# Kernel tuning notes

Measured on AMD Instinct MI355X. Metric: run time of the kernel, lower is better.

## Reference

```python
import jax, jax.numpy as jnp
import numpy as np

N = 50000      # neurons
R = 10         # max receptors per neuron
D = 5          # max delay (steps)
E = 10000000   # recurrent synapses
B = 1          # batch
DT = 1.0
LR_SCALE = 1.0
REC_DAMP = 0.4       # recurrent_dampening_factor
DAMPENING = 0.3      # dampening_factor (surrogate grad)


def setup_inputs() -> dict:
    key = jax.random.key(0)
    ks = jax.random.split(key, 20)
    inputs = jax.random.normal(ks[0], (B, R * N), jnp.float32) * 0.01
    z_buf = (jax.random.uniform(ks[1], (B, D * N)) < 0.02).astype(jnp.float32)
    v = jax.random.uniform(ks[2], (B, N), jnp.float32)
    r = jnp.zeros((B, N), jnp.float32)
    asc_1 = jax.random.normal(ks[3], (B, N), jnp.float32) * 0.01
    asc_2 = jax.random.normal(ks[4], (B, N), jnp.float32) * 0.01
    psc_rise = jax.random.uniform(ks[5], (B, R * N), jnp.float32) * 0.01
    psc = jax.random.uniform(ks[6], (B, R * N), jnp.float32) * 0.01
    rec_w = jax.random.normal(ks[7], (E,), jnp.float32) * 0.01
    rows = jax.random.randint(ks[8], (E,), 0, R * N, jnp.int32)
    cols = jax.random.randint(ks[9], (E,), 0, D * N, jnp.int32)
    rec_idx = jnp.stack([rows, cols], axis=1)
    # voltages are normalized by (V_th - E_L): v_th -> 1, e_l -> 0, v_reset -> 0
    v_th = jnp.ones((N,), jnp.float32)
    e_l = jnp.zeros((N,), jnp.float32)
    v_reset = jnp.zeros((N,), jnp.float32)
    g = jax.random.uniform(ks[10], (N,), jnp.float32, 3.0, 6.0)
    tau_m = jax.random.uniform(ks[11], (N,), jnp.float32, 5.0, 30.0)
    decay = jnp.exp(-DT / tau_m)
    current_factor = jax.random.uniform(ks[12], (N,), jnp.float32, 0.5, 1.5)
    t_ref = jnp.full((N,), 2.2, jnp.float32)
    k = jax.random.normal(ks[13], (N, 2), jnp.float32)  # stored in inv-sigmoid domain
    asc_amps = jax.random.normal(ks[14], (N, 2), jnp.float32) * 0.1
    tau_syn = jax.random.uniform(ks[15], (R * N,), jnp.float32, 2.0, 10.0)
    syn_decay = jnp.exp(-DT / tau_syn)
    psc_initial = jnp.asarray(np.e, jnp.float32) / tau_syn
    voltage_scale = jnp.full((N,), 30.0, jnp.float32)
    voltage_offset = jnp.full((N,), -70.0, jnp.float32)
    return dict(inputs=inputs, z_buf=z_buf, v=v, r=r, asc_1=asc_1, asc_2=asc_2,
                psc_rise=psc_rise, psc=psc, rec_w=rec_w, rec_idx=rec_idx,
                v_th=v_th, e_l=e_l, v_reset=v_reset, g=g, decay=decay,
                current_factor=current_factor, t_ref=t_ref, k=k, asc_amps=asc_amps,
                syn_decay=syn_decay, psc_initial=psc_initial,
                voltage_scale=voltage_scale, voltage_offset=voltage_offset)


def reference(inputs, z_buf, v, r, asc_1, asc_2, psc_rise, psc, rec_w, rec_idx,
              v_th, e_l, v_reset, g, decay, current_factor, t_ref, k, asc_amps,
              syn_decay, psc_initial, voltage_scale, voltage_offset):
    # one BillehColumn time step
    shaped = z_buf.reshape(B, D, N)          # (B, max_delay, N)
    prev_z = shaped[:, 0]
    # gradient-dampened spike buffer (fwd value identical to z_buf)
    dampened = z_buf * REC_DAMP
    rec_z = jax.lax.stop_gradient(z_buf - dampened) + dampened
    # sparse synaptic matmul: rows = neuron*R + receptor, cols = delay-slot neuron
    vals = rec_w[:, None] * rec_z.T[rec_idx[:, 1]]                       # (E, B)
    i_rec = jax.ops.segment_sum(vals, rec_idx[:, 0], num_segments=R * N).T  # (B, R*N)
    rec_inputs = i_rec * LR_SCALE + inputs
    # double-exponential synapse dynamics
    new_psc_rise = syn_decay * psc_rise + rec_inputs * psc_initial
    new_psc = psc * syn_decay + DT * syn_decay * psc_rise
    # refractory counter
    new_r = jnp.maximum(r + prev_z * t_ref - DT, 0.0)
    # after-spike currents (k stored in inv-sigmoid domain)
    kk = jax.nn.sigmoid(k)
    new_asc_1 = jnp.exp(-DT * kk[:, 0]) * asc_1 + prev_z * asc_amps[:, 0]
    new_asc_2 = jnp.exp(-DT * kk[:, 1]) * asc_2 + prev_z * asc_amps[:, 1]
    # membrane update: sum psc over receptors
    input_current = psc.reshape(B, N, R).sum(-1)
    new_v = decay * v + current_factor * (input_current + asc_1 + asc_2 + g * e_l)
    # surrogate-spike threshold (forward: heaviside)
    v_sc = (new_v - v_th) / (v_th - e_l)
    new_z = (v_sc > 0.0).astype(jnp.float32)
    new_z = jnp.where(new_r > 0.0, 0.0, new_z)
    # hard reset
    new_v = jnp.where(new_z > 0.5, jnp.broadcast_to(v_reset, new_v.shape), new_v)
    # shift delay buffer
    new_z_buf = jnp.concatenate([new_z[:, None], shaped[:, :-1]], axis=1).reshape(B, D * N)
    out_v = new_v * voltage_scale + voltage_offset
    return (new_z, out_v, new_z_buf, new_v, new_r, new_asc_1, new_asc_2,
            new_psc_rise, new_psc)
```

## Files before the change

kernel.cpp:

```cpp
#include <hip/hip_runtime.h>

namespace {

constexpr int N  = 50000;
constexpr int R  = 10;
constexpr int DD = 5;
constexpr int RN = R * N;
constexpr int DN = DD * N;
constexpr int E  = 10000000;
constexpr int EP = E / 2;
constexpr int EPH = EP / 2;

constexpr int ZB_BLOCKS = (DN + 255) / 256;
constexpr int ZB_WORDS  = ZB_BLOCKS * 256 / 32;

constexpr int SEED_BLOCKS = (RN / 4 + 255) / 256;
constexpr int NEUR_BLOCKS = (N + 255) / 256;
constexpr int PRE_BLOCKS  = ZB_BLOCKS + SEED_BLOCKS + NEUR_BLOCKS;

constexpr int SC_BLOCK = 512;
constexpr int SC_GRID  = 1024;

__global__ __launch_bounds__(256) void pre_kernel(
    const float*  __restrict__ z_buf,
    unsigned int* __restrict__ bits,
    const float4* __restrict__ inputs4,
    const float*  __restrict__ psc_rise,
    const float*  __restrict__ psc,
    const float*  __restrict__ syn_decay,
    const float*  __restrict__ psc_initial,
    const float*  __restrict__ v,
    const float*  __restrict__ r,
    const float*  __restrict__ asc1,
    const float*  __restrict__ asc2,
    const float*  __restrict__ v_th,
    const float*  __restrict__ e_l,
    const float*  __restrict__ v_reset,
    const float*  __restrict__ g,
    const float*  __restrict__ decay,
    const float*  __restrict__ current_factor,
    const float*  __restrict__ t_ref,
    const float2* __restrict__ k,
    const float2* __restrict__ asc_amps,
    const float*  __restrict__ voltage_scale,
    const float*  __restrict__ voltage_offset,
    float*        __restrict__ out)
{
    int b = blockIdx.x;
    int tid = threadIdx.x;

    if (b < ZB_BLOCKS) {
        int i = b * 256 + tid;
        float zv = (i < DN) ? z_buf[i] : 0.0f;
        unsigned long long m = __ballot(zv != 0.0f);
        if ((tid & 63) == 0) {
            int w = i >> 5;
            bits[w]     = (unsigned int)m;
            bits[w + 1] = (unsigned int)(m >> 32);
        }
        return;
    }
    b -= ZB_BLOCKS;
    if (b < SEED_BLOCKS) {
        int j = b * 256 + tid;
        if (j >= RN / 4) return;
        const float4* pr4 = reinterpret_cast<const float4*>(psc_rise);
        const float4* ps4 = reinterpret_cast<const float4*>(psc);
        const float4* sd4 = reinterpret_cast<const float4*>(syn_decay);
        const float4* pi4 = reinterpret_cast<const float4*>(psc_initial);
        float4* opr4 = reinterpret_cast<float4*>(out + 11 * N);
        float4* ops4 = reinterpret_cast<float4*>(out + 21 * N);
        float4 sd = sd4[j];
        float4 pr = pr4[j];
        float4 pi = pi4[j];
        float4 in = inputs4[j];
        float4 ps = ps4[j];
        float4 opr, ops;
        opr.x = sd.x * pr.x + in.x * pi.x;
        opr.y = sd.y * pr.y + in.y * pi.y;
        opr.z = sd.z * pr.z + in.z * pi.z;
        opr.w = sd.w * pr.w + in.w * pi.w;
        ops.x = ps.x * sd.x + sd.x * pr.x;
        ops.y = ps.y * sd.y + sd.y * pr.y;
        ops.z = ps.z * sd.z + sd.z * pr.z;
        ops.w = ps.w * sd.w + sd.w * pr.w;
        opr4[j] = opr;
        ops4[j] = ops;
        return;
    }
    b -= SEED_BLOCKS;
    {
        int n = b * 256 + tid;
        if (n >= N) return;

        float prev_z = z_buf[n];

        const float2* p2 = reinterpret_cast<const float2*>(psc + n * R);
        float ic = 0.0f;
#pragma unroll
        for (int t = 0; t < R / 2; ++t) {
            float2 pp = p2[t];
            ic += pp.x + pp.y;
        }

        float new_r = fmaxf(r[n] + prev_z * t_ref[n] - 1.0f, 0.0f);

        float2 kk = k[n];
        float2 aa = asc_amps[n];
        float s0 = 1.0f / (1.0f + expf(-kk.x));
        float s1 = 1.0f / (1.0f + expf(-kk.y));
        float a1_old = asc1[n];
        float a2_old = asc2[n];
        float new_a1 = expf(-s0) * a1_old + prev_z * aa.x;
        float new_a2 = expf(-s1) * a2_old + prev_z * aa.y;

        float el = e_l[n];
        float new_v = decay[n] * v[n]
                    + current_factor[n] * (ic + a1_old + a2_old + g[n] * el);

        float vth = v_th[n];
        float v_sc = (new_v - vth) / (vth - el);
        float nz = (v_sc > 0.0f) ? 1.0f : 0.0f;
        if (new_r > 0.0f) nz = 0.0f;
        if (nz > 0.5f) new_v = v_reset[n];

        out[0 * N + n]  = nz;
        out[1 * N + n]  = new_v * voltage_scale[n] + voltage_offset[n];
        out[2 * N + n]  = nz;
        out[7 * N + n]  = new_v;
        out[8 * N + n]  = new_r;
        out[9 * N + n]  = new_a1;
        out[10 * N + n] = new_a2;
    }
}

__device__ __forceinline__ void edge_pair(
    const int4 a, int p, const unsigned int* bits,
    const float* __restrict__ rec_w, const float* __restrict__ pinit,
    float* __restrict__ opr)
{
    unsigned int w0 = bits[a.y >> 5];
    unsigned int w1 = bits[a.w >> 5];
    if ((w0 >> (a.y & 31)) & 1u)
        atomicAdd(opr + a.x, rec_w[2 * p] * pinit[a.x]);
    if ((w1 >> (a.w & 31)) & 1u)
        atomicAdd(opr + a.z, rec_w[2 * p + 1] * pinit[a.z]);
}

__global__ __launch_bounds__(SC_BLOCK) void scatter_kernel(
    const float* __restrict__ rec_w,
    const int4*  __restrict__ idx4,
    const unsigned int* __restrict__ bits_g,
    const float* __restrict__ pinit,
    const float* __restrict__ z_buf,
    float*       __restrict__ out)
{
    __shared__ unsigned int bits[ZB_WORDS];
    {
        const uint4* src = reinterpret_cast<const uint4*>(bits_g);
        uint4* dst = reinterpret_cast<uint4*>(bits);
        for (int i = threadIdx.x; i < ZB_WORDS / 4; i += SC_BLOCK)
            dst[i] = src[i];
    }
    __syncthreads();

    float* opr = out + 11 * N;

    const int gs  = SC_GRID * SC_BLOCK;
    const int gid = blockIdx.x * SC_BLOCK + threadIdx.x;

    int pA = gid, pB = gid + EPH;
    bool hA = pA < EPH;
    bool hB = pB < EP;
    int4 a = {0, 0, 0, 0}, b = {0, 0, 0, 0};
    if (hA) a = idx4[pA];
    if (hB) b = idx4[pB];
    while (hA || hB) {
        int nA = pA + gs, nB = pB + gs;
        bool hnA = hA && (nA < EPH);
        bool hnB = hB && (nB < EP);
        int4 na = {0, 0, 0, 0}, nb = {0, 0, 0, 0};
        if (hnA) na = idx4[nA];
        if (hnB) nb = idx4[nB];
        if (hA) edge_pair(a, pA, bits, rec_w, pinit, opr);
        if (hB) edge_pair(b, pB, bits, rec_w, pinit, opr);
        a = na; pA = nA; hA = hnA;
        b = nb; pB = nB; hB = hnB;
    }

    {
        const float4* src = reinterpret_cast<const float4*>(z_buf);
        float4* dst = reinterpret_cast<float4*>(out + 3 * N);
        for (int i = gid; i < (DN - N) / 4; i += gs)
            dst[i] = src[i];
    }
}

}

extern "C" void kernel_launch(void* const* d_in, const int* in_sizes, int n_in,
                              void* d_out, int out_size, void* d_ws, size_t ws_size,
                              hipStream_t stream) {
    const float* inputs         = (const float*)d_in[0];
    const float* z_buf          = (const float*)d_in[1];
    const float* v              = (const float*)d_in[2];
    const float* r              = (const float*)d_in[3];
    const float* asc1           = (const float*)d_in[4];
    const float* asc2           = (const float*)d_in[5];
    const float* psc_rise       = (const float*)d_in[6];
    const float* psc            = (const float*)d_in[7];
    const float* rec_w          = (const float*)d_in[8];
    const int*   rec_idx        = (const int*)d_in[9];
    const float* v_th           = (const float*)d_in[10];
    const float* e_l            = (const float*)d_in[11];
    const float* v_reset        = (const float*)d_in[12];
    const float* g              = (const float*)d_in[13];
    const float* decay          = (const float*)d_in[14];
    const float* current_factor = (const float*)d_in[15];
    const float* t_ref          = (const float*)d_in[16];
    const float* k              = (const float*)d_in[17];
    const float* asc_amps       = (const float*)d_in[18];
    const float* syn_decay      = (const float*)d_in[19];
    const float* psc_initial    = (const float*)d_in[20];
    const float* voltage_scale  = (const float*)d_in[21];
    const float* voltage_offset = (const float*)d_in[22];

    float* out = (float*)d_out;
    unsigned int* bits = (unsigned int*)d_ws;

    pre_kernel<<<PRE_BLOCKS, 256, 0, stream>>>(
        z_buf, bits, (const float4*)inputs, psc_rise, psc, syn_decay,
        psc_initial, v, r, asc1, asc2, v_th, e_l, v_reset, g, decay,
        current_factor, t_ref, (const float2*)k, (const float2*)asc_amps,
        voltage_scale, voltage_offset, out);

    scatter_kernel<<<SC_GRID, SC_BLOCK, 0, stream>>>(
        rec_w, (const int4*)rec_idx, bits, psc_initial, z_buf, out);
}
```

Baseline: 33.12 us.

## Compact active edges into per-wave LDS queue before issuing atomics

Each wave now ballots the edges whose presynaptic spike bit is set and appends them into a shared-memory ring queue. It then flushes 64 entries at a time, so every lane does one atomicAdd with its rec_w and psc_initial gather. This targets lane divergence: with about 2% spike density, most lanes sit idle while a few perform scattered loads and atomics. The cost is extra LDS traffic, ballot and popcount work, and wave-level bookkeeping, and the loop is now fully unrolled with a fixed iteration count.

After: 35.56 us. +7.4%, slower.

```diff
diff --git a/kernel.cpp b/kernel.cpp
--- a/kernel.cpp
+++ b/kernel.cpp
@@ -20,6 +20,9 @@
 
 constexpr int SC_BLOCK = 512;
 constexpr int SC_GRID  = 1024;
+constexpr int GS       = SC_GRID * SC_BLOCK;
+constexpr int NITER    = (EPH + GS - 1) / GS;
+constexpr int QCAP     = 128;
 
 __global__ __launch_bounds__(256) void pre_kernel(
     const float*  __restrict__ z_buf,
@@ -134,19 +137,6 @@
     }
 }
 
-__device__ __forceinline__ void edge_pair(
-    const int4 a, int p, const unsigned int* bits,
-    const float* __restrict__ rec_w, const float* __restrict__ pinit,
-    float* __restrict__ opr)
-{
-    unsigned int w0 = bits[a.y >> 5];
-    unsigned int w1 = bits[a.w >> 5];
-    if ((w0 >> (a.y & 31)) & 1u)
-        atomicAdd(opr + a.x, rec_w[2 * p] * pinit[a.x]);
-    if ((w1 >> (a.w & 31)) & 1u)
-        atomicAdd(opr + a.z, rec_w[2 * p + 1] * pinit[a.z]);
-}
-
 __global__ __launch_bounds__(SC_BLOCK) void scatter_kernel(
     const float* __restrict__ rec_w,
     const int4*  __restrict__ idx4,
@@ -156,6 +146,7 @@
     float*       __restrict__ out)
 {
     __shared__ unsigned int bits[ZB_WORDS];
+    __shared__ uint2 queue[SC_BLOCK / 64][QCAP];
     {
         const uint4* src = reinterpret_cast<const uint4*>(bits_g);
         uint4* dst = reinterpret_cast<uint4*>(bits);
@@ -166,32 +157,70 @@
 
     float* opr = out + 11 * N;
 
-    const int gs  = SC_GRID * SC_BLOCK;
+    const int wv   = threadIdx.x >> 6;
+    const int lane = threadIdx.x & 63;
+    uint2* q = queue[wv];
+
+    unsigned int head = 0, tail = 0;
+
     const int gid = blockIdx.x * SC_BLOCK + threadIdx.x;
 
-    int pA = gid, pB = gid + EPH;
-    bool hA = pA < EPH;
-    bool hB = pB < EP;
-    int4 a = {0, 0, 0, 0}, b = {0, 0, 0, 0};
-    if (hA) a = idx4[pA];
-    if (hB) b = idx4[pB];
-    while (hA || hB) {
-        int nA = pA + gs, nB = pB + gs;
-        bool hnA = hA && (nA < EPH);
-        bool hnB = hB && (nB < EP);
-        int4 na = {0, 0, 0, 0}, nb = {0, 0, 0, 0};
-        if (hnA) na = idx4[nA];
-        if (hnB) nb = idx4[nB];
-        if (hA) edge_pair(a, pA, bits, rec_w, pinit, opr);
-        if (hB) edge_pair(b, pB, bits, rec_w, pinit, opr);
-        a = na; pA = nA; hA = hnA;
-        b = nb; pB = nB; hB = hnB;
+    auto enq = [&](unsigned int e, unsigned int row, bool act) {
+        unsigned long long mask = __ballot(act);
+        if (mask) {
+            unsigned int off = __builtin_amdgcn_mbcnt_hi(
+                (unsigned int)(mask >> 32),
+                __builtin_amdgcn_mbcnt_lo((unsigned int)mask, 0));
+            if (act) q[(tail + off) & (QCAP - 1)] = make_uint2(e, row);
+            tail += (unsigned int)__popcll(mask);
+        }
+    };
+    auto flush64 = [&]() {
+        uint2 ent = q[(head + lane) & (QCAP - 1)];
+        atomicAdd(opr + ent.y, rec_w[ent.x] * pinit[ent.y]);
+        head += 64;
+    };
+
+    int pA = gid;
+    int pB = gid + EPH;
+#pragma unroll
+    for (int it = 0; it < NITER; ++it) {
+        bool hA = pA < EPH;
+        bool hB = pB < EP;
+        int4 a = hA ? idx4[pA] : make_int4(0, 0, 0, 0);
+        int4 b = hB ? idx4[pB] : make_int4(0, 0, 0, 0);
+
+        bool a0 = hA && ((bits[a.y >> 5] >> (a.y & 31)) & 1u);
+        bool a1 = hA && ((bits[a.w >> 5] >> (a.w & 31)) & 1u);
+        bool b0 = hB && ((bits[b.y >> 5] >> (b.y & 31)) & 1u);
+        bool b1 = hB && ((bits[b.w >> 5] >> (b.w & 31)) & 1u);
+
+        enq(2u * pA,     (unsigned)a.x, a0);
+        if (tail - head >= 64) flush64();
+        enq(2u * pA + 1, (unsigned)a.z, a1);
+        if (tail - head >= 64) flush64();
+        enq(2u * pB,     (unsigned)b.x, b0);
+        if (tail - head >= 64) flush64();
+        enq(2u * pB + 1, (unsigned)b.z, b1);
+        if (tail - head >= 64) flush64();
+
+        pA += GS;
+        pB += GS;
+    }
+
+    while (tail - head >= 64) flush64();
+    {
+        unsigned int rem = tail - head;
+        if (lane < (int)rem) {
+            uint2 ent = q[(head + lane) & (QCAP - 1)];
+            atomicAdd(opr + ent.y, rec_w[ent.x] * pinit[ent.y]);
+        }
     }
 
     {
         const float4* src = reinterpret_cast<const float4*>(z_buf);
         float4* dst = reinterpret_cast<float4*>(out + 3 * N);
-        for (int i = gid; i < (DN - N) / 4; i += gs)
+        for (int i = gid; i < (DN - N) / 4; i += GS)
             dst[i] = src[i];
     }
 }
```
